# Performance work log

Hardware: AMD Instinct MI355X
Metric: run time of the kernel (lower is better)

Reference implementation:

```python
import jax, jax.numpy as jnp
import numpy as np

LEVELS = (1, 2, 4)
NHEAD = 4
LN_EPS = 1e-5


def _layernorm(x, g, b):
    m = jnp.mean(x, axis=-1, keepdims=True)
    v = jnp.mean((x - m) ** 2, axis=-1, keepdims=True)
    return (x - m) * jax.lax.rsqrt(v + LN_EPS) * g + b


def _spp_pool(x, starts, ends):
    # Exact AdaptiveAvgPool1d over per-proposal segments via inclusive-prefix-sum.
    # x: [B,C,T]; starts/ends: [B,P] int. Returns [B, P, C*sum(LEVELS)].
    B, C, T = x.shape
    P = starts.shape[1]
    xt = jnp.transpose(x, (0, 2, 1))  # [B,T,C]
    csum = jnp.concatenate([jnp.zeros((B, 1, C), x.dtype), jnp.cumsum(xt, axis=1)], axis=1)  # [B,T+1,C]
    n = ends - starts  # [B,P], always >= 1
    feats = []
    for L in LEVELS:
        i = jnp.arange(L)
        lo = (starts[..., None] + (i * n[..., None]) // L).reshape(B, P * L)
        hi = (starts[..., None] + ((i + 1) * n[..., None] + L - 1) // L).reshape(B, P * L)
        slo = jnp.take_along_axis(csum, lo[..., None], axis=1)  # [B,P*L,C]
        shi = jnp.take_along_axis(csum, hi[..., None], axis=1)
        mean = (shi - slo) / (hi - lo).astype(x.dtype)[..., None]
        # torch view(N, C*L) flattens [C,L] C-major -> transpose bins to last axis
        feats.append(mean.reshape(B, P, L, C).transpose(0, 1, 3, 2).reshape(B, P, C * L))
    return jnp.concatenate(feats, axis=-1)


def _encoder_layer(x, qkv_w, qkv_b, out_w, out_b, g1, b1, w1, bb1, w2, bb2, g2, b2):
    # Post-norm nn.TransformerEncoderLayer with exact-erf gelu, dropout=0 (eval)
    B, P, d = x.shape
    dh = d // NHEAD
    qkv = x @ qkv_w.T + qkv_b  # [B,P,3d]
    q, k, v = jnp.split(qkv, 3, axis=-1)
    sh = lambda t: t.reshape(B, P, NHEAD, dh).transpose(0, 2, 1, 3)  # [B,H,P,dh]
    q, k, v = sh(q), sh(k), sh(v)
    scale = 1.0 / float(np.sqrt(dh))
    attn = jax.nn.softmax(jnp.einsum('bhqd,bhkd->bhqk', q, k) * scale, axis=-1)
    o = jnp.einsum('bhqk,bhkd->bhqd', attn, v).transpose(0, 2, 1, 3).reshape(B, P, d)
    o = o @ out_w.T + out_b
    x = _layernorm(x + o, g1, b1)
    h = jax.nn.gelu(x @ w1.T + bb1, approximate=False) @ w2.T + bb2
    return _layernorm(x + h, g2, b2)


def _forward(x, proposal_boxes, proj_w, proj_b, pos_w1, pos_b1, pos_w2, pos_b2,
             qkv_w, qkv_b, out_w, out_b, ln1_g, ln1_b, ff1_w, ff1_b,
             ff2_w, ff2_b, ln2_g, ln2_b, cls_w, cls_b, det_w, det_b):
    B, C, T = x.shape
    P = proposal_boxes.shape[1]
    starts = jnp.clip(proposal_boxes[..., 0], 0, T - 1)
    ends = jnp.clip(proposal_boxes[..., 1], 1, T)
    ends = jnp.where(ends <= starts, jnp.minimum(starts + 1, T), ends)
    feats = _spp_pool(x, starts, ends)  # [B,P,spp_out_dim]
    s_f = proposal_boxes[..., 0].astype(x.dtype)
    e_f = proposal_boxes[..., 1].astype(x.dtype)
    centers = (s_f + e_f) / 2.0
    lengths = jnp.maximum(e_f - s_f, 1.0)
    pos_feat = jnp.stack([centers / T, lengths / T], axis=-1)  # [B,P,2]
    sort_idx = jnp.argsort(centers, axis=1)
    feats_s = jnp.take_along_axis(feats, sort_idx[..., None], axis=1)
    pos_emb = jax.nn.relu(pos_feat @ pos_w1.T + pos_b1) @ pos_w2.T + pos_b2
    pos_emb_s = jnp.take_along_axis(pos_emb, sort_idx[..., None], axis=1)
    tok = feats_s @ proj_w.T + proj_b + pos_emb_s  # [B,P,d]
    for l in range(qkv_w.shape[0]):
        tok = _encoder_layer(tok, qkv_w[l], qkv_b[l], out_w[l], out_b[l],
                             ln1_g[l], ln1_b[l], ff1_w[l], ff1_b[l],
                             ff2_w[l], ff2_b[l], ln2_g[l], ln2_b[l])
    inv = jnp.argsort(sort_idx, axis=1)
    ctx = jnp.take_along_axis(tok, inv[..., None], axis=1)  # [B,P,d]
    class_logits = ctx @ cls_w.T + cls_b  # [B,P,nc]
    det_logits = ctx @ det_w.T + det_b
    class_prob = jax.nn.softmax(class_logits, axis=2)
    det_prob = jax.nn.softmax(det_logits, axis=1)
    joint_prob = class_prob * det_prob
    video_prob = joint_prob.sum(axis=1)
    return video_prob, joint_prob, class_logits, det_logits, ctx


def setup_inputs() -> dict:
    key = jax.random.key(0)
    ks = jax.random.split(key, 32)
    B, C, T, P = 8, 512, 2048, 512
    d, dff, nc, nl = 512, 1024, 30, 2
    spp_out = C * sum(LEVELS)
    s = 0.02
    f32 = jnp.float32
    inp = {
        'x': jax.random.normal(ks[0], (B, C, T), f32),
        'proposal_boxes': jax.random.randint(ks[1], (B, P, 2), 0, T).astype(jnp.int32),
        'proj_w': jax.random.normal(ks[2], (d, spp_out), f32) * s,
        'proj_b': jnp.zeros((d,), f32),
        'pos_w1': jax.random.normal(ks[3], (d, 2), f32) * s,
        'pos_b1': jnp.zeros((d,), f32),
        'pos_w2': jax.random.normal(ks[4], (d, d), f32) * s,
        'pos_b2': jnp.zeros((d,), f32),
        'qkv_w': jax.random.normal(ks[5], (nl, 3 * d, d), f32) * s,
        'qkv_b': jnp.zeros((nl, 3 * d), f32),
        'out_w': jax.random.normal(ks[6], (nl, d, d), f32) * s,
        'out_b': jnp.zeros((nl, d), f32),
        'ln1_g': jnp.ones((nl, d), f32),
        'ln1_b': jnp.zeros((nl, d), f32),
        'ff1_w': jax.random.normal(ks[7], (nl, dff, d), f32) * s,
        'ff1_b': jnp.zeros((nl, dff), f32),
        'ff2_w': jax.random.normal(ks[8], (nl, d, dff), f32) * s,
        'ff2_b': jnp.zeros((nl, d), f32),
        'ln2_g': jnp.ones((nl, d), f32),
        'ln2_b': jnp.zeros((nl, d), f32),
        'cls_w': jax.random.normal(ks[9], (nc, d), f32) * s,
        'cls_b': jnp.zeros((nc,), f32),
        'det_w': jax.random.normal(ks[10], (nc, d), f32) * s,
        'det_b': jnp.zeros((nc,), f32),
    }
    return inp


def reference(x, proposal_boxes, proj_w, proj_b, pos_w1, pos_b1, pos_w2, pos_b2,
              qkv_w, qkv_b, out_w, out_b, ln1_g, ln1_b, ff1_w, ff1_b,
              ff2_w, ff2_b, ln2_g, ln2_b, cls_w, cls_b, det_w, det_b):
    return _forward(x, proposal_boxes, proj_w, proj_b, pos_w1, pos_b1, pos_w2, pos_b2,
                    qkv_w, qkv_b, out_w, out_b, ln1_g, ln1_b, ff1_w, ff1_b,
                    ff2_w, ff2_b, ln2_g, ln2_b, cls_w, cls_b, det_w, det_b)
```

## Files before the change

### kernel.cpp

```cpp
#include <hip/hip_runtime.h>

#define TDIM 2048
#define CDIM 512
#define BDIM 8
#define PDIM 512
#define DMODEL 512
#define NCOUT 30
#define SPPOUT 3584
#define AKDIM 4096

typedef __attribute__((ext_vector_type(8))) short short8;
typedef __attribute__((ext_vector_type(4))) float f32x4;

typedef const __attribute__((address_space(1))) void* as1cv;
typedef __attribute__((address_space(3))) void* as3v;

__device__ __forceinline__ void gl_lds16(const short* g, short* l){
  __builtin_amdgcn_global_load_lds((as1cv)g, (as3v)l, 16, 0, 0);
}

__device__ __forceinline__ short f2b(float f){
  unsigned u = __float_as_uint(f);
  unsigned r = (u + 0x7fffu + ((u >> 16) & 1u)) >> 16;
  return (short)r;
}

__device__ __forceinline__ float waveSum(float v){
#pragma unroll
  for (int o = 32; o > 0; o >>= 1) v += __shfl_xor(v, o);
  return v;
}
__device__ __forceinline__ float waveMax(float v){
#pragma unroll
  for (int o = 32; o > 0; o >>= 1) v = fmaxf(v, __shfl_xor(v, o));
  return v;
}

__global__ void kzero(float* p, int n){
  int i = blockIdx.x * 256 + threadIdx.x;
  if (i < n) p[i] = 0.f;
}

__global__ void kprep2(const float* __restrict__ pw, const float* __restrict__ pw2,
                       const float* __restrict__ qw, const float* __restrict__ ow,
                       const float* __restrict__ f1, const float* __restrict__ f2,
                       const float* __restrict__ cl, const float* __restrict__ dt,
                       const float* __restrict__ pb, const float* __restrict__ pb2,
                       const float* __restrict__ cb, const float* __restrict__ db,
                       short* __restrict__ Wc, short* __restrict__ Wd,
                       float* __restrict__ bc, float* __restrict__ bh){
  int i = blockIdx.x * 256 + threadIdx.x;
  if (i < 2097152){
    int r = i >> 12, k = i & 4095;
    float v = (k < SPPOUT) ? pw[(size_t)r * SPPOUT + k] : pw2[(size_t)r * DMODEL + (k - SPPOUT)];
    Wc[i] = f2b(v);
  } else if (i < 6322176){
    int j = i - 2097152;
    float v;
    if (j < 1572864) v = qw[j];
    else if (j < 2097152) v = ow[j - 1572864];
    else if (j < 3145728) v = f1[j - 2097152];
    else if (j < 4194304) v = f2[j - 3145728];
    else if (j < 4209664) v = cl[j - 4194304];
    else v = dt[j - 4209664];
    Wd[j] = f2b(v);
  } else {
    int k = i - 6322176;
    if (k < 512) bc[k] = pb[k] + pb2[k];
    else if (k < 572) bh[k - 512] = (k < 542) ? cb[k - 512] : db[k - 542];
  }
}

__global__ void kscan(const float* __restrict__ x, float* __restrict__ W, float* __restrict__ tot){
  int idx = blockIdx.x;
  int b = idx >> 5, rem = idx & 31, ch = rem >> 1, cg = rem & 1;
  int c = cg * 256 + threadIdx.x;
  const float* xp = x + ((size_t)(b * CDIM + c)) * TDIM + ch * 128;
  float* wp = W + ((size_t)b * TDIM + ch * 128) * CDIM + c;
  float run = 0.f;
  for (int tl = 0; tl < 128; tl += 4){
    float4 v = *(const float4*)(xp + tl);
    run += v.x; wp[(size_t)(tl + 0) * CDIM] = run;
    run += v.y; wp[(size_t)(tl + 1) * CDIM] = run;
    run += v.z; wp[(size_t)(tl + 2) * CDIM] = run;
    run += v.w; wp[(size_t)(tl + 3) * CDIM] = run;
  }
  tot[((size_t)b * 16 + ch) * CDIM + c] = run;
}

__global__ void koff(const float* __restrict__ tot, float* __restrict__ off){
  int b = blockIdx.x >> 1, cg = blockIdx.x & 1;
  int c = cg * 256 + threadIdx.x;
  float run = 0.f;
  for (int ch = 0; ch < 16; ++ch){
    off[((size_t)b * 16 + ch) * CDIM + c] = run;
    run += tot[((size_t)b * 16 + ch) * CDIM + c];
  }
}

__global__ void ksort(const int* __restrict__ boxes, int* __restrict__ sidx){
  __shared__ unsigned key[PDIM];
  int b = blockIdx.x, t = threadIdx.x;
  int s = boxes[(size_t)(b * PDIM + t) * 2];
  int e = boxes[(size_t)(b * PDIM + t) * 2 + 1];
  key[t] = ((unsigned)(s + e) << 9) | (unsigned)t;
  __syncthreads();
  for (int k = 2; k <= PDIM; k <<= 1){
    for (int j = k >> 1; j > 0; j >>= 1){
      int ixj = t ^ j;
      if (ixj > t){
        unsigned a = key[t], c2 = key[ixj];
        bool up = ((t & k) == 0);
        bool doswap = up ? (a > c2) : (a < c2);
        if (doswap){ key[t] = c2; key[ixj] = a; }
      }
      __syncthreads();
    }
  }
  sidx[b * PDIM + t] = (int)(key[t] & 511u);
}

__global__ void kspp(const float* __restrict__ W, const float* __restrict__ off,
                     const int* __restrict__ boxes, const int* __restrict__ sidx,
                     const float* __restrict__ pw1, const float* __restrict__ pb1,
                     short* __restrict__ A){
  int blk = blockIdx.x;
  int b = blk >> 9, j = blk & 511;
  int p = sidx[b * PDIM + j];
  int s0 = boxes[(size_t)(b * PDIM + p) * 2];
  int e0 = boxes[(size_t)(b * PDIM + p) * 2 + 1];
  int start = min(max(s0, 0), TDIM - 1);
  int end   = min(max(e0, 1), TDIM);
  if (end <= start) end = min(start + 1, TDIM);
  int n = end - start;

  int lo[7], hi[7], cb[7], cl[7];
  {
    const int Ls[3] = {1, 2, 4};
    const int Bo[3] = {0, 512, 1536};
    int q = 0;
    for (int li = 0; li < 3; ++li){
      int L = Ls[li];
      for (int i = 0; i < L; ++i){
        lo[q] = start + (i * n) / L;
        hi[q] = start + ((i + 1) * n + L - 1) / L;
        cb[q] = Bo[li] + i;
        cl[q] = L;
        ++q;
      }
    }
  }
  float s_f = (float)s0, e_f = (float)e0;
  float px = (s_f + e_f) * 0.5f / (float)TDIM;
  float py = fmaxf(e_f - s_f, 1.f) / (float)TDIM;
  short* Ar = A + (size_t)(b * PDIM + j) * AKDIM;
  const float* Wb = W + (size_t)b * TDIM * CDIM;
  const float* ob = off + (size_t)b * 16 * CDIM;
  for (int c = threadIdx.x; c < CDIM; c += 256){
#pragma unroll
    for (int q = 0; q < 7; ++q){
      int l = lo[q], h = hi[q];
      float fl = (l == 0) ? 0.f : (Wb[(size_t)(l - 1) * CDIM + c] + ob[((l - 1) >> 7) * CDIM + c]);
      float fh = Wb[(size_t)(h - 1) * CDIM + c] + ob[((h - 1) >> 7) * CDIM + c];
      Ar[cb[q] + c * cl[q]] = f2b((fh - fl) / (float)(h - l));
    }
    float hv = pw1[c * 2] * px + pw1[c * 2 + 1] * py + pb1[c];
    Ar[SPPOUT + c] = f2b(fmaxf(hv, 0.f));
  }
}

template<int BN>
__global__ __launch_bounds__(256) void gemm_bt(
    int M, int N, int K,
    const short* __restrict__ A, int lda, long long sAb, long long sAh,
    const short* __restrict__ B, int ldb, long long sBb, long long sBh,
    float* __restrict__ Cf, short* __restrict__ Cb, int ldc, long long sCb, long long sCh,
    int hdiv, float alpha,
    const float* __restrict__ bias, const float* __restrict__ resid, int act)
{
  constexpr int JF = BN / 32;
  __shared__ short As[128 * 64];
  __shared__ short Bs[BN * 64];
  int z = blockIdx.z;
  int zb = z / hdiv, zh = z - zb * hdiv;
  A += (size_t)zb * sAb + (size_t)zh * sAh;
  B += (size_t)zb * sBb + (size_t)zh * sBh;
  size_t coff = (size_t)zb * sCb + (size_t)zh * sCh;
  int rowBase = blockIdx.y * 128, colBase = blockIdx.x * BN;
  int t = threadIdx.x;
  int lane = t & 63;
  int wave = t >> 6;
  int wm = (wave >> 1) * 64, wn = (wave & 1) * (BN / 2);
  int lm = lane & 15, quad = lane >> 4;
  int srow = t >> 3;
  int skw = ((t & 7) * 8) ^ ((srow & 7) * 8);

  const short* Agp[4];
#pragma unroll
  for (int it = 0; it < 4; ++it)
    Agp[it] = A + (size_t)min(rowBase + srow + it * 32, M - 1) * lda + skw;
  const short* Bgp[JF];
#pragma unroll
  for (int it = 0; it < JF; ++it)
    Bgp[it] = B + (size_t)min(colBase + srow + it * 32, N - 1) * ldb + skw;

  f32x4 zero4 = {0.f, 0.f, 0.f, 0.f};
  f32x4 acc[4][JF];
#pragma unroll
  for (int i = 0; i < 4; ++i)
#pragma unroll
    for (int j = 0; j < JF; ++j) acc[i][j] = zero4;

  int axr = (lm & 7) * 8;
  for (int k0 = 0; k0 < K; k0 += 64){
#pragma unroll
    for (int it = 0; it < 4; ++it) gl_lds16(Agp[it] + k0, As + it * 2048 + t * 8);
#pragma unroll
    for (int it = 0; it < JF; ++it) gl_lds16(Bgp[it] + k0, Bs + it * 2048 + t * 8);
    __syncthreads();
#pragma unroll
    for (int h = 0; h < 2; ++h){
      int koff = (h * 32 + quad * 8) ^ axr;
      short8 af[4], bfr[JF];
#pragma unroll
      for (int i = 0; i < 4; ++i)
        af[i] = *(const short8*)(As + (wm + i * 16 + lm) * 64 + koff);
#pragma unroll
      for (int j = 0; j < JF; ++j)
        bfr[j] = *(const short8*)(Bs + (wn + j * 16 + lm) * 64 + koff);
#pragma unroll
      for (int i = 0; i < 4; ++i)
#pragma unroll
        for (int j = 0; j < JF; ++j)
          acc[i][j] = __builtin_amdgcn_mfma_f32_16x16x32_bf16(af[i], bfr[j], acc[i][j], 0, 0, 0);
    }
    __syncthreads();
  }

#pragma unroll
  for (int i = 0; i < 4; ++i){
#pragma unroll
    for (int j = 0; j < JF; ++j){
#pragma unroll
      for (int r = 0; r < 4; ++r){
        int row = rowBase + wm + i * 16 + quad * 4 + r;
        int col = colBase + wn + j * 16 + lm;
        if (row < M && col < N){
          float v = acc[i][j][r] * alpha;
          if (bias) v += bias[col];
          size_t ci = coff + (size_t)row * ldc + col;
          if (resid) v += resid[ci];
          if (act) v = 0.5f * v * (1.f + erff(v * 0.7071067811865476f));
          if (Cf) Cf[ci] = v;
          if (Cb) Cb[ci] = f2b(v);
        }
      }
    }
  }
}

__global__ void kredG1(const float* __restrict__ part, const float* __restrict__ bias,
                       float* __restrict__ tok, short* __restrict__ tokb){
  int i = blockIdx.x * 256 + threadIdx.x;
  float v = part[i] + part[i + 2097152] + part[i + 4194304] + part[i + 6291456] + bias[i & 511];
  tok[i] = v;
  tokb[i] = f2b(v);
}

__global__ void kredPV(const float* __restrict__ part, short* __restrict__ ob){
  int i = blockIdx.x * 256 + threadIdx.x;
  int n = i & 127;
  int h = (i >> 7) & 3;
  int q = (i >> 9) & 511;
  int b = i >> 18;
  int src = (((b << 2) + h) << 16) + (q << 7) + n;
  ob[i] = f2b(part[src] + part[src + 2097152]);
}

__global__ void klnR(const float* __restrict__ part, const float* __restrict__ bias,
                     const float* __restrict__ resid,
                     const float* __restrict__ g, const float* __restrict__ bb,
                     float* __restrict__ Yf, short* __restrict__ Yb){
  int row = blockIdx.x, lane = threadIdx.x;
  size_t base = (size_t)row * DMODEL;
  float v[8]; float s = 0.f;
#pragma unroll
  for (int i = 0; i < 8; ++i){
    int c = lane + 64 * i;
    v[i] = part[base + c] + part[base + c + 2097152] + bias[c] + resid[base + c];
    s += v[i];
  }
  s = waveSum(s);
  float m = s * (1.f / DMODEL);
  float q = 0.f;
#pragma unroll
  for (int i = 0; i < 8; ++i){ float d = v[i] - m; q += d * d; }
  q = waveSum(q);
  float inv = rsqrtf(q * (1.f / DMODEL) + 1e-5f);
#pragma unroll
  for (int i = 0; i < 8; ++i){
    int c = lane + 64 * i;
    float o = (v[i] - m) * inv * g[c] + bb[c];
    Yf[base + c] = o;
    Yb[base + c] = f2b(o);
  }
}

__global__ void kattn(const float* __restrict__ S, short* __restrict__ Sb,
                      const short* __restrict__ qkvb, short* __restrict__ Vt){
  __shared__ short T[32][33];
  int blk = blockIdx.x, t = threadIdx.x;
  if (blk < 4096){
    int row = blk * 4 + (t >> 6), lane = t & 63;
    const float* p = S + (size_t)row * 512;
    short* q = Sb + (size_t)row * 512;
    float v[8]; float m = -1e30f;
#pragma unroll
    for (int i = 0; i < 8; ++i){ v[i] = p[lane + 64 * i]; m = fmaxf(m, v[i]); }
    m = waveMax(m);
    float s = 0.f;
#pragma unroll
    for (int i = 0; i < 8; ++i){ v[i] = expf(v[i] - m); s += v[i]; }
    s = waveSum(s);
    float r = 1.f / s;
#pragma unroll
    for (int i = 0; i < 8; ++i) q[lane + 64 * i] = f2b(v[i] * r);
  } else {
    int bid = blk - 4096;
    int bh = bid >> 6, pt = (bid >> 2) & 15, nt = bid & 3;
    int b = bh >> 2, h = bh & 3;
    int tx = t & 31, ty = t >> 5;
    const short* src = qkvb + (size_t)(b * 512) * 1536 + 1024 + h * 128;
    int p0 = pt * 32, n0 = nt * 32;
#pragma unroll
    for (int q = 0; q < 4; ++q)
      T[ty * 4 + q][tx] = src[(size_t)(p0 + ty * 4 + q) * 1536 + n0 + tx];
    __syncthreads();
    short* dst = Vt + (size_t)bh * 128 * 512;
#pragma unroll
    for (int q = 0; q < 4; ++q)
      dst[(size_t)(n0 + ty * 4 + q) * 512 + p0 + tx] = T[tx][ty * 4 + q];
  }
}

__global__ void kdetsm(const float* __restrict__ hd, float* __restrict__ dp){
  int b = blockIdx.x / NCOUT, c = blockIdx.x % NCOUT, lane = threadIdx.x;
  float v[8]; float m = -1e30f;
#pragma unroll
  for (int i = 0; i < 8; ++i){
    v[i] = hd[((size_t)(b * PDIM) + lane + 64 * i) * 60 + 30 + c];
    m = fmaxf(m, v[i]);
  }
  m = waveMax(m);
  float s = 0.f;
#pragma unroll
  for (int i = 0; i < 8; ++i){ v[i] = expf(v[i] - m); s += v[i]; }
  s = waveSum(s);
  float r = 1.f / s;
#pragma unroll
  for (int i = 0; i < 8; ++i)
    dp[((size_t)(b * PDIM) + lane + 64 * i) * NCOUT + c] = v[i] * r;
}

__global__ void kfinal(const float* __restrict__ hd, const float* __restrict__ dps,
                       const float* __restrict__ tok, const int* __restrict__ sidx,
                       float* __restrict__ out){
  int blk = blockIdx.x;
  int b = blk >> 9, j = blk & 511;
  int lane = threadIdx.x;
  int p = sidx[b * PDIM + j];
  float* video = out;
  float* joint = out + 240;
  float* clso  = out + 123120;
  float* deto  = out + 246000;
  float* ctxo  = out + 368880;
  size_t rs60 = (size_t)(b * PDIM + j) * 60;
  size_t rs30 = (size_t)(b * PDIM + j) * NCOUT;
  size_t ro = (size_t)(b * PDIM + p) * NCOUT;
  float lc = (lane < NCOUT) ? hd[rs60 + lane] : -1e30f;
  float m = waveMax(lc);
  float e = (lane < NCOUT) ? expf(lc - m) : 0.f;
  float s = waveSum(e);
  float cp = e / s;
  if (lane < NCOUT){
    float dv  = hd[rs60 + 30 + lane];
    float dpv = dps[rs30 + lane];
    float jp  = cp * dpv;
    clso[ro + lane] = lc;
    deto[ro + lane] = dv;
    joint[ro + lane] = jp;
    atomicAdd(&video[b * NCOUT + lane], jp);
  }
  const float* tr = tok + (size_t)(b * PDIM + j) * DMODEL;
  float* cr = ctxo + (size_t)(b * PDIM + p) * DMODEL;
  for (int c = lane; c < DMODEL; c += 64) cr[c] = tr[c];
}

extern "C" void kernel_launch(void* const* d_in, const int* in_sizes, int n_in,
                              void* d_out, int out_size, void* d_ws, size_t ws_size,
                              hipStream_t stream) {
  const float* x      = (const float*)d_in[0];
  const int*   boxes  = (const int*)d_in[1];
  const float* proj_w = (const float*)d_in[2];
  const float* proj_b = (const float*)d_in[3];
  const float* pos_w1 = (const float*)d_in[4];
  const float* pos_b1 = (const float*)d_in[5];
  const float* pos_w2 = (const float*)d_in[6];
  const float* pos_b2 = (const float*)d_in[7];
  const float* qkv_w  = (const float*)d_in[8];
  const float* qkv_b  = (const float*)d_in[9];
  const float* out_w  = (const float*)d_in[10];
  const float* out_b  = (const float*)d_in[11];
  const float* ln1_g  = (const float*)d_in[12];
  const float* ln1_b  = (const float*)d_in[13];
  const float* ff1_w  = (const float*)d_in[14];
  const float* ff1_b  = (const float*)d_in[15];
  const float* ff2_w  = (const float*)d_in[16];
  const float* ff2_b  = (const float*)d_in[17];
  const float* ln2_g  = (const float*)d_in[18];
  const float* ln2_b  = (const float*)d_in[19];
  const float* cls_w  = (const float*)d_in[20];
  const float* cls_b  = (const float*)d_in[21];
  const float* det_w  = (const float*)d_in[22];
  const float* det_b  = (const float*)d_in[23];
  float* out = (float*)d_out;
  float* ws  = (float*)d_ws;

  const size_t oR1    = 0;
  const size_t oS     = 9437184;
  const size_t oSbf   = 17825792;
  const size_t oTok   = 22020096;
  const size_t oTokb  = 24117248;
  const size_t oTok2  = 25165824;
  const size_t oTok2b = 27262976;
  const size_t oWcat  = 28311552;
  const size_t oBcat  = 29360128;
  const size_t oWq    = 29360640;
  const size_t oWo    = 30147072;
  const size_t oWf1   = 30409216;
  const size_t oWf2   = 30933504;
  const size_t oWcls  = 31457792;
  const size_t oTot   = 31473152;
  const size_t oOff   = 31538688;
  const size_t oSidx  = 31604224;
  const size_t oBhead = oTot;

  short* Abf   = (short*)(ws + oR1);
  short* qkvb  = (short*)(ws + oR1);
  short* Vt    = (short*)(ws + oR1 + 3145728);
  short* obufb = (short*)(ws + oR1 + 4194304);
  short* hbufb = (short*)(ws + oR1 + 5242880);
  float* headS = ws + oR1 + 7340032;
  float* dpS   = ws + oR1 + 7585792;
  float* csum  = ws + oS;
  float* Cpart = ws + oS;
  float* S     = ws + oS;
  float* Cp2   = ws + oS;
  short* Sbf   = (short*)(ws + oSbf);
  float* tok   = ws + oTok;
  short* tokb  = (short*)(ws + oTokb);
  float* tok2  = ws + oTok2;
  short* tok2b = (short*)(ws + oTok2b);
  short* Wcatb = (short*)(ws + oWcat);
  float* bcat  = ws + oBcat;
  short* Wq    = (short*)(ws + oWq);
  short* Wo    = (short*)(ws + oWo);
  short* Wf1   = (short*)(ws + oWf1);
  short* Wf2   = (short*)(ws + oWf2);
  short* Whead = (short*)(ws + oWcls);
  float* tot   = ws + oTot;
  float* offp  = ws + oOff;
  int*   sidx  = (int*)(ws + oSidx);
  float* bhead = ws + oBhead;

  kzero<<<1, 256, 0, stream>>>(out, 240);
  kscan<<<256, 256, 0, stream>>>(x, csum, tot);
  koff<<<16, 256, 0, stream>>>(tot, offp);
  ksort<<<BDIM, 512, 0, stream>>>(boxes, sidx);
  kprep2<<<24699, 256, 0, stream>>>(proj_w, pos_w2, qkv_w, out_w, ff1_w, ff2_w, cls_w, det_w,
                                    proj_b, pos_b2, cls_b, det_b, Wcatb, Wq, bcat, bhead);
  kspp<<<BDIM * PDIM, 256, 0, stream>>>(csum, offp, boxes, sidx, pos_w1, pos_b1, Abf);

  gemm_bt<64><<<dim3(8, 32, 4), 256, 0, stream>>>(
      4096, 512, 1024, Abf, 4096, 1024, 0, Wcatb, 4096, 1024, 0,
      Cpart, nullptr, 512, 2097152, 0, 1, 1.f, nullptr, nullptr, 0);
  kredG1<<<8192, 256, 0, stream>>>(Cpart, bcat, tok, tokb);

  const float scale = 0.08838834764831845f;
  for (int l = 0; l < 2; ++l){
    const short* qw  = Wq  + (size_t)l * 1536 * 512;
    const short* ow  = Wo  + (size_t)l * 512 * 512;
    const short* f1w = Wf1 + (size_t)l * 1024 * 512;
    const short* f2w = Wf2 + (size_t)l * 512 * 1024;
    const float* qb  = qkv_b + (size_t)l * 1536;
    const float* obv = out_b + (size_t)l * 512;
    const float* f1b = ff1_b + (size_t)l * 1024;
    const float* f2b_ = ff2_b + (size_t)l * 512;

    gemm_bt<64><<<dim3(24, 32, 1), 256, 0, stream>>>(
        4096, 1536, 512, tokb, 512, 0, 0, qw, 512, 0, 0,
        nullptr, qkvb, 1536, 0, 0, 1, 1.f, qb, nullptr, 0);
    gemm_bt<128><<<dim3(4, 4, 32), 256, 0, stream>>>(
        512, 512, 128,
        qkvb, 1536, (long long)512 * 1536, 128,
        qkvb + 512, 1536, (long long)512 * 1536, 128,
        S, nullptr, 512, (long long)4 * 512 * 512, (long long)512 * 512,
        4, scale, nullptr, nullptr, 0);
    kattn<<<6144, 256, 0, stream>>>(S, Sbf, qkvb, Vt);
    gemm_bt<64><<<dim3(2, 4, 64), 256, 0, stream>>>(
        512, 128, 256,
        Sbf, 512, 256, (long long)512 * 512,
        Vt, 512, 256, (long long)128 * 512,
        Cp2, nullptr, 128, 2097152, (long long)512 * 128,
        32, 1.f, nullptr, nullptr, 0);
    kredPV<<<8192, 256, 0, stream>>>(Cp2, obufb);
    gemm_bt<64><<<dim3(8, 32, 2), 256, 0, stream>>>(
        4096, 512, 256, obufb, 512, 256, 0, ow, 512, 256, 0,
        Cp2, nullptr, 512, 2097152, 0, 1, 1.f, nullptr, nullptr, 0);
    klnR<<<4096, 64, 0, stream>>>(Cp2, obv, tok, ln1_g + l * 512, ln1_b + l * 512, tok2, tok2b);
    gemm_bt<64><<<dim3(16, 32, 1), 256, 0, stream>>>(
        4096, 1024, 512, tok2b, 512, 0, 0, f1w, 512, 0, 0,
        nullptr, hbufb, 1024, 0, 0, 1, 1.f, f1b, nullptr, 1);
    gemm_bt<64><<<dim3(8, 32, 2), 256, 0, stream>>>(
        4096, 512, 512, hbufb, 1024, 512, 0, f2w, 1024, 512, 0,
        Cp2, nullptr, 512, 2097152, 0, 1, 1.f, nullptr, nullptr, 0);
    klnR<<<4096, 64, 0, stream>>>(Cp2, f2b_, tok2, ln2_g + l * 512, ln2_b + l * 512, tok, tokb);
  }

  gemm_bt<64><<<dim3(1, 32, 1), 256, 0, stream>>>(
      4096, 60, 512, tokb, 512, 0, 0, Whead, 512, 0, 0,
      headS, nullptr, 60, 0, 0, 1, 1.f, bhead, nullptr, 0);
  kdetsm<<<BDIM * NCOUT, 64, 0, stream>>>(headS, dpS);
  kfinal<<<BDIM * PDIM, 64, 0, stream>>>(headS, dpS, tok, sidx, out);
}
```

Before: 549.7 us.

## Fuse attention into a flash-style kernel and swizzle first GEMM block order

Replaces the separate QK^T GEMM, softmax, and split-K PV GEMM with its reduction by one fused online-softmax attention kernel. It uses MFMA and reads K and the transposed V directly from global memory. This avoids writing and re-reading the fp32 score matrix and its bf16 copy. The change also remaps block indices in the first projection GEMM for better cache locality, and folds output zeroing into the sort kernel to drop one launch. The risk is that the flash kernel launches only 256 blocks, has no LDS staging for K and V, and may be latency bound.

Result: no change. 543.8 us (-1.1%).

```diff
diff --git a/kernel.cpp b/kernel.cpp
--- a/kernel.cpp
+++ b/kernel.cpp
@@ -34,11 +34,6 @@
 #pragma unroll
   for (int o = 32; o > 0; o >>= 1) v = fmaxf(v, __shfl_xor(v, o));
   return v;
-}
-
-__global__ void kzero(float* p, int n){
-  int i = blockIdx.x * 256 + threadIdx.x;
-  if (i < n) p[i] = 0.f;
 }
 
 __global__ void kprep2(const float* __restrict__ pw, const float* __restrict__ pw2,
@@ -98,9 +93,10 @@
   }
 }
 
-__global__ void ksort(const int* __restrict__ boxes, int* __restrict__ sidx){
+__global__ void ksort(const int* __restrict__ boxes, int* __restrict__ sidx, float* __restrict__ out){
   __shared__ unsigned key[PDIM];
   int b = blockIdx.x, t = threadIdx.x;
+  if (b == 0 && t < 240) out[t] = 0.f;
   int s = boxes[(size_t)(b * PDIM + t) * 2];
   int e = boxes[(size_t)(b * PDIM + t) * 2 + 1];
   key[t] = ((unsigned)(s + e) << 9) | (unsigned)t;
@@ -169,7 +165,7 @@
   }
 }
 
-template<int BN>
+template<int BN, int SWZ = 0>
 __global__ __launch_bounds__(256) void gemm_bt(
     int M, int N, int K,
     const short* __restrict__ A, int lda, long long sAb, long long sAh,
@@ -181,12 +177,19 @@
   constexpr int JF = BN / 32;
   __shared__ short As[128 * 64];
   __shared__ short Bs[BN * 64];
-  int z = blockIdx.z;
-  int zb = z / hdiv, zh = z - zb * hdiv;
+  int bx = blockIdx.x, by = blockIdx.y, bz = blockIdx.z;
+  if constexpr (SWZ){
+    int flat = (bz * 32 + by) * 8 + bx;
+    int wl = flat >> 3;
+    by = (flat & 7) * 4 + (wl & 3);
+    bx = (wl >> 2) & 7;
+    bz = wl >> 5;
+  }
+  int zb = bz / hdiv, zh = bz - zb * hdiv;
   A += (size_t)zb * sAb + (size_t)zh * sAh;
   B += (size_t)zb * sBb + (size_t)zh * sBh;
   size_t coff = (size_t)zb * sCb + (size_t)zh * sCh;
-  int rowBase = blockIdx.y * 128, colBase = blockIdx.x * BN;
+  int rowBase = by * 128, colBase = bx * BN;
   int t = threadIdx.x;
   int lane = t & 63;
   int wave = t >> 6;
@@ -267,14 +270,116 @@
   tokb[i] = f2b(v);
 }
 
-__global__ void kredPV(const float* __restrict__ part, short* __restrict__ ob){
-  int i = blockIdx.x * 256 + threadIdx.x;
-  int n = i & 127;
-  int h = (i >> 7) & 3;
-  int q = (i >> 9) & 511;
-  int b = i >> 18;
-  int src = (((b << 2) + h) << 16) + (q << 7) + n;
-  ob[i] = f2b(part[src] + part[src + 2097152]);
+__global__ void kvt(const short* __restrict__ qkvb, short* __restrict__ Vt){
+  __shared__ short T[32][33];
+  int bh = blockIdx.x, pt = blockIdx.y, nt = blockIdx.z;
+  int b = bh >> 2, h = bh & 3;
+  int tx = threadIdx.x, ty = threadIdx.y;
+  const short* src = qkvb + (size_t)(b * 512) * 1536 + 1024 + h * 128;
+  int p0 = pt * 32, n0 = nt * 32;
+#pragma unroll
+  for (int q = 0; q < 4; ++q)
+    T[ty * 4 + q][tx] = src[(size_t)(p0 + ty * 4 + q) * 1536 + n0 + tx];
+  __syncthreads();
+  short* dst = Vt + (size_t)bh * 128 * 512;
+#pragma unroll
+  for (int q = 0; q < 4; ++q)
+    dst[(size_t)(n0 + ty * 4 + q) * 512 + p0 + tx] = T[tx][ty * 4 + q];
+}
+
+__global__ __launch_bounds__(256) void kflash(const short* __restrict__ qkvb,
+                                              const short* __restrict__ Vt,
+                                              short* __restrict__ ob){
+  __shared__ short P[4][1024];
+  int bid = blockIdx.x;
+  int bh = bid & 31, qt = bid >> 5;
+  int b = bh >> 2, h = bh & 3;
+  int t = threadIdx.x;
+  int w = t >> 6, lane = t & 63;
+  int lm = lane & 15, quad = lane >> 4;
+  const float scale = 0.08838834764831845f;
+
+  const short* qbase = qkvb + (size_t)(b * 512 + qt * 64 + w * 16 + lm) * 1536 + h * 128 + quad * 8;
+  short8 qf[4];
+#pragma unroll
+  for (int s = 0; s < 4; ++s) qf[s] = *(const short8*)(qbase + s * 32);
+
+  const short* kbase = qkvb + (size_t)(b * 512) * 1536 + 512 + h * 128 + quad * 8;
+  const short* vbase = Vt + (size_t)bh * 65536 + (size_t)lm * 512 + quad * 8;
+
+  f32x4 zero4 = {0.f, 0.f, 0.f, 0.f};
+  f32x4 Of[8];
+#pragma unroll
+  for (int i = 0; i < 8; ++i) Of[i] = zero4;
+  float mrun[4] = {-1e30f, -1e30f, -1e30f, -1e30f};
+  float lrun[4] = {0.f, 0.f, 0.f, 0.f};
+  short* Pw = &P[w][0];
+
+  for (int kt = 0; kt < 8; ++kt){
+    f32x4 Sf[4];
+#pragma unroll
+    for (int j = 0; j < 4; ++j) Sf[j] = zero4;
+#pragma unroll
+    for (int s = 0; s < 4; ++s){
+#pragma unroll
+      for (int j = 0; j < 4; ++j){
+        short8 kf = *(const short8*)(kbase + (size_t)(kt * 64 + j * 16 + lm) * 1536 + s * 32);
+        Sf[j] = __builtin_amdgcn_mfma_f32_16x16x32_bf16(qf[s], kf, Sf[j], 0, 0, 0);
+      }
+    }
+    float alpha[4];
+#pragma unroll
+    for (int r = 0; r < 4; ++r){
+      float mx = fmaxf(fmaxf(Sf[0][r], Sf[1][r]), fmaxf(Sf[2][r], Sf[3][r])) * scale;
+#pragma unroll
+      for (int o = 1; o < 16; o <<= 1) mx = fmaxf(mx, __shfl_xor(mx, o));
+      float mnew = fmaxf(mrun[r], mx);
+      alpha[r] = expf(mrun[r] - mnew);
+      float psum = 0.f;
+#pragma unroll
+      for (int j = 0; j < 4; ++j){
+        float p = expf(Sf[j][r] * scale - mnew);
+        Sf[j][r] = p;
+        psum += p;
+      }
+#pragma unroll
+      for (int o = 1; o < 16; o <<= 1) psum += __shfl_xor(psum, o);
+      lrun[r] = lrun[r] * alpha[r] + psum;
+      mrun[r] = mnew;
+    }
+#pragma unroll
+    for (int i = 0; i < 8; ++i)
+#pragma unroll
+      for (int r = 0; r < 4; ++r) Of[i][r] *= alpha[r];
+#pragma unroll
+    for (int j = 0; j < 4; ++j)
+#pragma unroll
+      for (int r = 0; r < 4; ++r){
+        int q = quad * 4 + r;
+        int key = j * 16 + lm;
+        Pw[q * 64 + (key ^ ((q & 7) * 8))] = f2b(Sf[j][r]);
+      }
+#pragma unroll
+    for (int ts = 0; ts < 2; ++ts){
+      short8 pa = *(const short8*)(Pw + lm * 64 + (((ts * 32 + quad * 8) ^ ((lm & 7) * 8))));
+#pragma unroll
+      for (int jd = 0; jd < 8; ++jd){
+        short8 vf = *(const short8*)(vbase + (size_t)(jd * 16) * 512 + kt * 64 + ts * 32);
+        Of[jd] = __builtin_amdgcn_mfma_f32_16x16x32_bf16(pa, vf, Of[jd], 0, 0, 0);
+      }
+    }
+  }
+  float inv[4];
+#pragma unroll
+  for (int r = 0; r < 4; ++r) inv[r] = 1.f / lrun[r];
+  int qg = qt * 64 + w * 16 + quad * 4;
+#pragma unroll
+  for (int jd = 0; jd < 8; ++jd)
+#pragma unroll
+    for (int r = 0; r < 4; ++r){
+      size_t ci = ((size_t)(b * 512 + qg + r)) * 512 + h * 128 + jd * 16 + lm;
+      ob[ci] = f2b(Of[jd][r] * inv[r]);
+    }
 }
 
 __global__ void klnR(const float* __restrict__ part, const float* __restrict__ bias,
@@ -303,43 +408,6 @@
     float o = (v[i] - m) * inv * g[c] + bb[c];
     Yf[base + c] = o;
     Yb[base + c] = f2b(o);
-  }
-}
-
-__global__ void kattn(const float* __restrict__ S, short* __restrict__ Sb,
-                      const short* __restrict__ qkvb, short* __restrict__ Vt){
-  __shared__ short T[32][33];
-  int blk = blockIdx.x, t = threadIdx.x;
-  if (blk < 4096){
-    int row = blk * 4 + (t >> 6), lane = t & 63;
-    const float* p = S + (size_t)row * 512;
-    short* q = Sb + (size_t)row * 512;
-    float v[8]; float m = -1e30f;
-#pragma unroll
-    for (int i = 0; i < 8; ++i){ v[i] = p[lane + 64 * i]; m = fmaxf(m, v[i]); }
-    m = waveMax(m);
-    float s = 0.f;
-#pragma unroll
-    for (int i = 0; i < 8; ++i){ v[i] = expf(v[i] - m); s += v[i]; }
-    s = waveSum(s);
-    float r = 1.f / s;
-#pragma unroll
-    for (int i = 0; i < 8; ++i) q[lane + 64 * i] = f2b(v[i] * r);
-  } else {
-    int bid = blk - 4096;
-    int bh = bid >> 6, pt = (bid >> 2) & 15, nt = bid & 3;
-    int b = bh >> 2, h = bh & 3;
-    int tx = t & 31, ty = t >> 5;
-    const short* src = qkvb + (size_t)(b * 512) * 1536 + 1024 + h * 128;
-    int p0 = pt * 32, n0 = nt * 32;
-#pragma unroll
-    for (int q = 0; q < 4; ++q)
-      T[ty * 4 + q][tx] = src[(size_t)(p0 + ty * 4 + q) * 1536 + n0 + tx];
-    __syncthreads();
-    short* dst = Vt + (size_t)bh * 128 * 512;
-#pragma unroll
-    for (int q = 0; q < 4; ++q)
-      dst[(size_t)(n0 + ty * 4 + q) * 512 + p0 + tx] = T[tx][ty * 4 + q];
   }
 }
 
@@ -428,7 +496,6 @@
 
   const size_t oR1    = 0;
   const size_t oS     = 9437184;
-  const size_t oSbf   = 17825792;
   const size_t oTok   = 22020096;
   const size_t oTokb  = 24117248;
   const size_t oTok2  = 25165824;
@@ -454,9 +521,7 @@
   float* dpS   = ws + oR1 + 7585792;
   float* csum  = ws + oS;
   float* Cpart = ws + oS;
-  float* S     = ws + oS;
   float* Cp2   = ws + oS;
-  short* Sbf   = (short*)(ws + oSbf);
   float* tok   = ws + oTok;
   short* tokb  = (short*)(ws + oTokb);
   float* tok2  = ws + oTok2;
@@ -473,20 +538,18 @@
   int*   sidx  = (int*)(ws + oSidx);
   float* bhead = ws + oBhead;
 
-  kzero<<<1, 256, 0, stream>>>(out, 240);
   kscan<<<256, 256, 0, stream>>>(x, csum, tot);
   koff<<<16, 256, 0, stream>>>(tot, offp);
-  ksort<<<BDIM, 512, 0, stream>>>(boxes, sidx);
+  ksort<<<BDIM, 512, 0, stream>>>(boxes, sidx, out);
   kprep2<<<24699, 256, 0, stream>>>(proj_w, pos_w2, qkv_w, out_w, ff1_w, ff2_w, cls_w, det_w,
                                     proj_b, pos_b2, cls_b, det_b, Wcatb, Wq, bcat, bhead);
   kspp<<<BDIM * PDIM, 256, 0, stream>>>(csum, offp, boxes, sidx, pos_w1, pos_b1, Abf);
 
-  gemm_bt<64><<<dim3(8, 32, 4), 256, 0, stream>>>(
+  gemm_bt<64, 1><<<dim3(8, 32, 4), 256, 0, stream>>>(
       4096, 512, 1024, Abf, 4096, 1024, 0, Wcatb, 4096, 1024, 0,
       Cpart, nullptr, 512, 2097152, 0, 1, 1.f, nullptr, nullptr, 0);
   kredG1<<<8192, 256, 0, stream>>>(Cpart, bcat, tok, tokb);
 
-  const float scale = 0.08838834764831845f;
   for (int l = 0; l < 2; ++l){
     const short* qw  = Wq  + (size_t)l * 1536 * 512;
     const short* ow  = Wo  + (size_t)l * 512 * 512;
@@ -500,20 +563,8 @@
     gemm_bt<64><<<dim3(24, 32, 1), 256, 0, stream>>>(
         4096, 1536, 512, tokb, 512, 0, 0, qw, 512, 0, 0,
         nullptr, qkvb, 1536, 0, 0, 1, 1.f, qb, nullptr, 0);
-    gemm_bt<128><<<dim3(4, 4, 32), 256, 0, stream>>>(
-        512, 512, 128,
-        qkvb, 1536, (long long)512 * 1536, 128,
-        qkvb + 512, 1536, (long long)512 * 1536, 128,
-        S, nullptr, 512, (long long)4 * 512 * 512, (long long)512 * 512,
-        4, scale, nullptr, nullptr, 0);
-    kattn<<<6144, 256, 0, stream>>>(S, Sbf, qkvb, Vt);
-    gemm_bt<64><<<dim3(2, 4, 64), 256, 0, stream>>>(
-        512, 128, 256,
-        Sbf, 512, 256, (long long)512 * 512,
-        Vt, 512, 256, (long long)128 * 512,
-        Cp2, nullptr, 128, 2097152, (long long)512 * 128,
-        32, 1.f, nullptr, nullptr, 0);
-    kredPV<<<8192, 256, 0, stream>>>(Cp2, obufb);
+    kvt<<<dim3(32, 16, 4), dim3(32, 8), 0, stream>>>(qkvb, Vt);
+    kflash<<<256, 256, 0, stream>>>(qkvb, Vt, obufb);
     gemm_bt<64><<<dim3(8, 32, 2), 256, 0, stream>>>(
         4096, 512, 256, obufb, 512, 256, 0, ow, 512, 256, 0,
         Cp2, nullptr, 512, 2097152, 0, 1, 1.f, nullptr, nullptr, 0);
```
